# Kernel tuning notes

Hardware: AMD Instinct MI355X
Metric: run time of the kernel (lower is better)

The kernel has to match this reference:

```python
import jax, jax.numpy as jnp
import numpy as np

N_NODES = 100000
N_EDGES = 3200000
IN_FEAT = 128
HIDDEN = 32
NUM_LAYERS = 4
K = 35
NODES_PER_GRAPH = 100


def setup_inputs() -> dict:
    key = jax.random.key(0)
    ks = jax.random.split(key, 20)
    inp = {}
    inp['x'] = jax.random.normal(ks[0], (N_NODES, IN_FEAT), dtype=jnp.float32)
    inp['edge_index'] = jax.random.randint(ks[1], (2, N_EDGES), 0, N_NODES, dtype=jnp.int64)
    inp['batch'] = (jnp.arange(N_NODES, dtype=jnp.int64) // NODES_PER_GRAPH)
    # GCNConv weights (PyG: lin weight [in, out], bias [out])
    dims = [IN_FEAT] + [HIDDEN] * NUM_LAYERS
    for i in range(NUM_LAYERS):
        s = 1.0 / np.sqrt(dims[i])
        inp[f'w{i}'] = jax.random.normal(ks[2 + i], (dims[i], HIDDEN), dtype=jnp.float32) * s
        inp[f'b{i}'] = jnp.zeros((HIDDEN,), dtype=jnp.float32)
    # head: Conv1d(128->16,k=1), Conv1d(16->32,k=5), fc1(416->128), fc2(128->1)
    inp['conv1_w'] = jax.random.normal(ks[8], (16, HIDDEN * NUM_LAYERS, 1), dtype=jnp.float32) * (1.0 / np.sqrt(128))
    inp['conv1_b'] = jnp.zeros((16,), dtype=jnp.float32)
    inp['conv2_w'] = jax.random.normal(ks[9], (32, 16, 5), dtype=jnp.float32) * (1.0 / np.sqrt(16 * 5))
    inp['conv2_b'] = jnp.zeros((32,), dtype=jnp.float32)
    lin_in = 32 * (K // 2 - 4)  # 416
    inp['fc1_w'] = jax.random.normal(ks[10], (128, lin_in), dtype=jnp.float32) * (1.0 / np.sqrt(lin_in))
    inp['fc1_b'] = jnp.zeros((128,), dtype=jnp.float32)
    inp['fc2_w'] = jax.random.normal(ks[11], (1, 128), dtype=jnp.float32) * (1.0 / np.sqrt(128))
    inp['fc2_b'] = jnp.zeros((1,), dtype=jnp.float32)
    return inp


def _gcn_conv(x, w, b, src, dst, n):
    # PyG GCNConv: h = x @ W; add self-loops; sym-normalized scatter-add; + bias
    h = x @ w
    deg = jnp.ones((n,), h.dtype).at[dst].add(1.0)  # degree incl. self-loop
    dis = jax.lax.rsqrt(deg)
    coef = dis[src] * dis[dst]  # [E]
    agg = jax.ops.segment_sum(h[src] * coef[:, None], dst, num_segments=n)
    return agg + h / deg[:, None] + b  # self-loop norm = 1/deg


def reference(x, edge_index, batch, w0, b0, w1, b1, w2, b2, w3, b3,
              conv1_w, conv1_b, conv2_w, conv2_b, fc1_w, fc1_b, fc2_w, fc2_b):
    src, dst = edge_index[0], edge_index[1]
    n = x.shape[0]
    xs = []
    h = x
    for w, b in ((w0, b0), (w1, b1), (w2, b2), (w3, b3)):
        h = jnp.tanh(_gcn_conv(h, w, b, src, dst, n))
        xs.append(h)
    feat = jnp.concatenate(xs, axis=1)  # [N, 128]
    # global_sort_pool: graphs are contiguous blocks of NODES_PER_GRAPH nodes
    G = n // NODES_PER_GRAPH
    dense = feat.reshape(G, NODES_PER_GRAPH, -1)
    order = jnp.argsort(-dense[:, :, -1], axis=1)  # descending by last channel
    topk = jnp.take_along_axis(dense, order[:, :, None], axis=1)[:, :K]  # [G,K,128]
    y = topk.transpose(0, 2, 1)  # [G,128,K]
    y = jax.nn.relu(jnp.einsum('oc,gck->gok', conv1_w[:, :, 0], y) + conv1_b[None, :, None])
    L = y.shape[-1] // 2  # MaxPool1d(2), drop trailing element
    y = y[..., :L * 2].reshape(G, 16, L, 2).max(axis=-1)  # [G,16,17]
    y = jax.lax.conv_general_dilated(y, conv2_w, (1,), 'VALID',
                                     dimension_numbers=('NCH', 'OIH', 'NCH'))
    y = jax.nn.relu(y + conv2_b[None, :, None])  # [G,32,13]
    y = y.reshape(G, -1)  # [G,416]
    y = jax.nn.relu(y @ fc1_w.T + fc1_b)  # dropout is identity in eval
    return jax.nn.sigmoid(y @ fc2_w.T + fc2_b)  # [G,1]
```

## Files before the change

kernel.cpp:

```cpp
#include <hip/hip_runtime.h>
#include <hip/hip_fp16.h>
#include <math.h>

#define N_NODES 100000
#define N_EDGES 3200000
#define HIDDEN 32
#define K_TOP 35
#define NPG 100
#define N_GRAPHS 1000

#define BSHIFT 9
#define NLOC 512
#define NBUCK 196
#define CAP 17408
#define NBB 1024
#define BIN_CHUNK 13


__global__ void k_bin(const int* __restrict__ src, const int* __restrict__ dst,
                      int* __restrict__ bcnt, unsigned int* __restrict__ bdata) {
    __shared__ int h[NBUCK];
    __shared__ int lbase[NBUCK];
    __shared__ int lcur[NBUCK];
    int t = threadIdx.x;
    for (int i = t; i < NBUCK; i += 256) { h[i] = 0; lcur[i] = 0; }
    __syncthreads();
    int base = blockIdx.x * (256 * BIN_CHUNK);
    int ss[BIN_CHUNK], ds[BIN_CHUNK];
#pragma unroll
    for (int k = 0; k < BIN_CHUNK; k++) {
        int e = base + k * 256 + t;
        if (e < N_EDGES) {
            ss[k] = src[e];
            ds[k] = dst[e];
            atomicAdd(&h[ds[k] >> BSHIFT], 1);
        } else ds[k] = -1;
    }
    __syncthreads();
    for (int i = t; i < NBUCK; i += 256)
        lbase[i] = h[i] ? atomicAdd(&bcnt[i], h[i]) : 0;
    __syncthreads();
#pragma unroll
    for (int k = 0; k < BIN_CHUNK; k++) {
        int d = ds[k];
        if (d >= 0) {
            int bk = d >> BSHIFT;
            int pos = atomicAdd(&lcur[bk], 1);
            bdata[bk * CAP + lbase[bk] + pos] =
                ((unsigned int)ss[k] << BSHIFT) | (unsigned int)(d & (NLOC - 1));
        }
    }
}

__global__ void k_build(const unsigned int* __restrict__ bdata, const int* __restrict__ bcnt,
                        int2* __restrict__ rc, float* __restrict__ dis,
                        int* __restrict__ csr) {
    __shared__ int h[NLOC];
    __shared__ int sd[NLOC];
    __shared__ int rp[NLOC];
    __shared__ int cur[NLOC];
    int b = blockIdx.x, t = threadIdx.x;
    if (t < NLOC) h[t] = 0;
    __syncthreads();
    int r0 = b * CAP, r1 = r0 + bcnt[b];
    for (int i = r0 + t; i < r1; i += 1024)
        atomicAdd(&h[bdata[i] & (NLOC - 1)], 1);
    __syncthreads();
    int v = (t < NLOC) ? h[t] : 0;
    if (t < NLOC) sd[t] = v;
    __syncthreads();
    for (int off = 1; off < NLOC; off <<= 1) {
        int x = (t >= off && t < NLOC) ? sd[t - off] : 0;
        __syncthreads();
        if (t < NLOC) sd[t] += x;
        __syncthreads();
    }
    if (t < NLOC) {
        int excl = sd[t] - v;
        int node = (b << BSHIFT) + t;
        rp[t] = r0 + excl;
        cur[t] = 0;
        if (node < N_NODES) {
            rc[node] = make_int2(r0 + excl, v);
            dis[node] = rsqrtf((float)(v + 1));
        }
    }
    __syncthreads();
    for (int i = r0 + t; i < r1; i += 1024) {
        unsigned int u = bdata[i];
        int loc = u & (NLOC - 1);
        int pos = atomicAdd(&cur[loc], 1);
        csr[rp[loc] + pos] = (int)(u >> BSHIFT);
    }
}


__global__ void k_mm0(const float* __restrict__ in, const float* __restrict__ w,
                      const float* __restrict__ dis, char* __restrict__ hs) {
    __shared__ float wl[128 * HIDDEN];
    int t = threadIdx.x;
    for (int i = t; i < 128 * HIDDEN; i += 256) wl[i] = w[i];
    __syncthreads();
    int n0 = blockIdx.x * 512 + t;
    int n1 = n0 + 256;
    bool has0 = n0 < N_NODES, has1 = n1 < N_NODES;
    int m0 = has0 ? n0 : 0, m1 = has1 ? n1 : 0;
    const float* r0p = in + (size_t)m0 * 128;
    const float* r1p = in + (size_t)m1 * 128;
    float acc0[HIDDEN], acc1[HIDDEN];
#pragma unroll
    for (int o = 0; o < HIDDEN; o++) { acc0[o] = 0.f; acc1[o] = 0.f; }
    for (int c4 = 0; c4 < 32; c4++) {
        float4 va = *(const float4*)(r0p + c4 * 4);
        float4 vb = *(const float4*)(r1p + c4 * 4);
        float xa[4] = {va.x, va.y, va.z, va.w};
        float xb[4] = {vb.x, vb.y, vb.z, vb.w};
#pragma unroll
        for (int k = 0; k < 4; k++) {
            const float* wr = &wl[(c4 * 4 + k) * HIDDEN];
#pragma unroll
            for (int o = 0; o < HIDDEN; o++) {
                float wv = wr[o];
                acc0[o] += xa[k] * wv;
                acc1[o] += xb[k] * wv;
            }
        }
    }
    if (has0) {
        float d = dis[m0];
        float4* hr = (float4*)(hs + (size_t)m0 * 64);
#pragma unroll
        for (int qq = 0; qq < 4; qq++) {
            __half2 p[4];
#pragma unroll
            for (int k = 0; k < 4; k++)
                p[k] = __floats2half2_rn(acc0[8 * qq + 2 * k] * d, acc0[8 * qq + 2 * k + 1] * d);
            hr[qq] = *(float4*)p;
        }
    }
    if (has1) {
        float d = dis[m1];
        float4* hr = (float4*)(hs + (size_t)m1 * 64);
#pragma unroll
        for (int qq = 0; qq < 4; qq++) {
            __half2 p[4];
#pragma unroll
            for (int k = 0; k < 4; k++)
                p[k] = __floats2half2_rn(acc1[8 * qq + 2 * k] * d, acc1[8 * qq + 2 * k + 1] * d);
            hr[qq] = *(float4*)p;
        }
    }
}

__global__ void k_agg(const float4* __restrict__ hs4, const float* __restrict__ dis,
                      const int2* __restrict__ rc, const int* __restrict__ csr_src,
                      const float* __restrict__ bias,
                      float* __restrict__ feat, int col_off,
                      const float* __restrict__ wnext, char* __restrict__ hsn) {
    __shared__ float wl[32 * 33];
    __shared__ float tv[8][36];
    int tt = threadIdx.x;
    if (wnext) {
        for (int i = tt; i < 1024; i += 256)
            wl[(i >> 5) * 33 + (i & 31)] = wnext[i];
    }
    __syncthreads();
    int n = (blockIdx.x * 256 + tt) >> 5;
    int c = tt & 31;
    int r = c & 3;
    int ph = c >> 2;
    int slot = tt >> 5;
    int2 rcv = rc[n];
    int start = rcv.x, m = rcv.y;
    float d = dis[n];
    float aA[8] = {0.f, 0.f, 0.f, 0.f, 0.f, 0.f, 0.f, 0.f};
    float aB[8] = {0.f, 0.f, 0.f, 0.f, 0.f, 0.f, 0.f, 0.f};

    for (int base = 0; base < m; base += 32) {
        int e = base + c;
        int idx = (e < m) ? csr_src[start + e] : N_NODES;
        int id0 = __shfl(idx, ph, 32);
        int id1 = __shfl(idx, 8 + ph, 32);
        int id2 = __shfl(idx, 16 + ph, 32);
        int id3 = __shfl(idx, 24 + ph, 32);
        float4 g0 = hs4[(size_t)id0 * 4 + r];
        float4 g1 = hs4[(size_t)id1 * 4 + r];
        float4 g2 = hs4[(size_t)id2 * 4 + r];
        float4 g3 = hs4[(size_t)id3 * 4 + r];
        const __half2* h0 = (const __half2*)&g0;
        const __half2* h1 = (const __half2*)&g1;
        const __half2* h2 = (const __half2*)&g2;
        const __half2* h3 = (const __half2*)&g3;
        float2 f;
#pragma unroll
        for (int j = 0; j < 4; j++) {
            f = __half22float2(h0[j]); aA[2 * j] += f.x; aA[2 * j + 1] += f.y;
        }
#pragma unroll
        for (int j = 0; j < 4; j++) {
            f = __half22float2(h1[j]); aB[2 * j] += f.x; aB[2 * j + 1] += f.y;
        }
#pragma unroll
        for (int j = 0; j < 4; j++) {
            f = __half22float2(h2[j]); aA[2 * j] += f.x; aA[2 * j + 1] += f.y;
        }
#pragma unroll
        for (int j = 0; j < 4; j++) {
            f = __half22float2(h3[j]); aB[2 * j] += f.x; aB[2 * j + 1] += f.y;
        }
    }
    float s[8];
#pragma unroll
    for (int k = 0; k < 8; k++) {
        float v = aA[k] + aB[k];
        v += __shfl_xor(v, 4);
        v += __shfl_xor(v, 8);
        v += __shfl_xor(v, 16);
        s[k] = v;
    }
    float s01 = (ph & 1) ? s[1] : s[0];
    float s23 = (ph & 1) ? s[3] : s[2];
    float s45 = (ph & 1) ? s[5] : s[4];
    float s67 = (ph & 1) ? s[7] : s[6];
    float s03 = (ph & 2) ? s23 : s01;
    float s47 = (ph & 2) ? s67 : s45;
    float sp  = (ph & 4) ? s47 : s03;
    float4 sv = hs4[(size_t)n * 4 + r];
    const __half2* sh = (const __half2*)&sv;
    __half2 q01 = (ph & 2) ? sh[1] : sh[0];
    __half2 q23 = (ph & 2) ? sh[3] : sh[2];
    __half2 qq  = (ph & 4) ? q23 : q01;
    float self = (ph & 1) ? __high2float(qq) : __low2float(qq);
    float bv = bias[8 * r + ph];
    float ov = tanhf(d * (sp + self) + bv);
    __builtin_nontemporal_store(ov, &feat[(size_t)n * 128 + col_off + 8 * r + ph]);
    if (wnext) {
        tv[slot][8 * r + ph] = ov;
        __builtin_amdgcn_wave_barrier();
        float o = 0.f;
#pragma unroll 8
        for (int k = 0; k < 32; k++)
            o += tv[slot][k] * wl[k * 33 + c];
        o *= d;
        float oh = __shfl_xor(o, 1);
        if ((c & 1) == 0) {
            __half2 pck = __floats2half2_rn(o, oh);
            *(__half2*)(hsn + (size_t)n * 64 + (size_t)c * 2) = pck;
        }
    }
}


__global__ void __launch_bounds__(256, 4)
k_head(const float* __restrict__ feat,
       const float* __restrict__ c1w, const float* __restrict__ c1b,
       const float* __restrict__ c2w, const float* __restrict__ c2b,
       const float* __restrict__ f1w, const float* __restrict__ f1b,
       const float* __restrict__ f2w, const float* __restrict__ f2b,
       float* __restrict__ out) {
    __shared__ float vals[NPG];
    __shared__ int sel[K_TOP];
    __shared__ float tk[K_TOP * 132];
    __shared__ float wl1[16 * 129];
    __shared__ float y1[16][36];
    __shared__ float y2[16][17];
    __shared__ float y3[416];
    __shared__ float y4[128];
    __shared__ float r2[128];
    int g = blockIdx.x, t = threadIdx.x;
    const float* fg = feat + (size_t)g * NPG * 128;

    for (int i = t; i < 2048; i += 256)
        wl1[(i >> 7) * 129 + (i & 127)] = c1w[i];
    if (t < NPG) vals[t] = fg[t * 128 + 127];
    __syncthreads();
    if (t < NPG) {
        float v = vals[t];
        int r = 0;
        for (int j = 0; j < NPG; j++) {
            float u = vals[j];
            r += (u > v) || (u == v && j < t);
        }
        if (r < K_TOP) sel[r] = t;
    }
    __syncthreads();
    for (int i = t; i < K_TOP * 32; i += 256) {
        int k = i >> 5, c4 = i & 31;
        *(float4*)&tk[k * 132 + 4 * c4] = *(const float4*)&fg[sel[k] * 128 + 4 * c4];
    }
    __syncthreads();
    for (int i = t; i < 16 * K_TOP; i += 256) {
        int o = i & 15, k = i >> 4;
        float s = c1b[o];
        const float* wr = &wl1[o * 129];
        const float* xr = &tk[k * 132];
#pragma unroll 8
        for (int c = 0; c < 128; c++) s += wr[c] * xr[c];
        y1[o][k] = fmaxf(s, 0.f);
    }
    __syncthreads();
    for (int i = t; i < 16 * 17; i += 256) {
        int o = i & 15, l = i >> 4;
        y2[o][l] = fmaxf(y1[o][2 * l], y1[o][2 * l + 1]);
    }
    __syncthreads();
    for (int idx = t; idx < 32 * 13; idx += 256) {
        int o2 = idx / 13, ttp = idx - o2 * 13;
        float s = c2b[o2];
        const float* wr = c2w + o2 * 80;
#pragma unroll
        for (int i = 0; i < 16; i++)
#pragma unroll
            for (int j = 0; j < 5; j++) s += wr[i * 5 + j] * y2[i][ttp + j];
        y3[idx] = fmaxf(s, 0.f);
    }
    __syncthreads();
    {
        int o = t >> 1, h = t & 1;
        const float4* wr4 = (const float4*)(f1w + o * 416) + h * 52;
        const float* yb = y3 + h * 208;
        float s = 0.f;
#pragma unroll 4
        for (int i = 0; i < 52; i++) {
            float4 w4 = wr4[i];
            s += w4.x * yb[4 * i] + w4.y * yb[4 * i + 1] +
                 w4.z * yb[4 * i + 2] + w4.w * yb[4 * i + 3];
        }
        s += __shfl_xor(s, 1);
        if (h == 0) y4[o] = fmaxf(s + f1b[o], 0.f);
    }
    __syncthreads();
    if (t < 128) r2[t] = f2w[t] * y4[t];
    __syncthreads();
    for (int off = 64; off > 0; off >>= 1) {
        if (t < off) r2[t] += r2[t + off];
        __syncthreads();
    }
    if (t == 0) out[g] = 1.0f / (1.0f + expf(-(r2[0] + f2b[0])));
}


static inline size_t alignup(size_t x) { return (x + 255) & ~(size_t)255; }

extern "C" void kernel_launch(void* const* d_in, const int* in_sizes, int n_in,
                              void* d_out, int out_size, void* d_ws, size_t ws_size,
                              hipStream_t stream) {
    const float* x    = (const float*)d_in[0];
    const int*   ei   = (const int*)d_in[1];
    const int*   srcp = ei;
    const int*   dstp = ei + N_EDGES;
    const float* w0 = (const float*)d_in[3];
    const float* b0 = (const float*)d_in[4];
    const float* w1 = (const float*)d_in[5];
    const float* b1 = (const float*)d_in[6];
    const float* w2 = (const float*)d_in[7];
    const float* b2 = (const float*)d_in[8];
    const float* w3 = (const float*)d_in[9];
    const float* b3 = (const float*)d_in[10];
    const float* c1w = (const float*)d_in[11];
    const float* c1b = (const float*)d_in[12];
    const float* c2w = (const float*)d_in[13];
    const float* c2b = (const float*)d_in[14];
    const float* f1w = (const float*)d_in[15];
    const float* f1b = (const float*)d_in[16];
    const float* f2w = (const float*)d_in[17];
    const float* f2b = (const float*)d_in[18];
    float* out = (float*)d_out;

    char* p = (char*)d_ws;
    int2* rcv    = (int2*)p; p += alignup(sizeof(int2) * N_NODES);
    float* dis   = (float*)p; p += alignup(sizeof(float) * N_NODES);
    int* bcnt    = (int*)p; p += alignup(sizeof(int) * NBUCK);
    int* csr     = (int*)p; p += alignup(sizeof(int) * (size_t)NBUCK * CAP);
    char* U = p;
    unsigned int* bdata = (unsigned int*)U;
    char* hsA = U;
    char* hsB = U + alignup((size_t)N_NODES * 64 + 64);
    size_t usz = alignup(sizeof(unsigned int) * (size_t)NBUCK * CAP);
    float* feat = (float*)(U + usz);

    const int NB_M = (N_NODES + 511) / 512;
    const int NB_A = (N_NODES * 32) / 256;

    hipMemsetAsync(bcnt, 0, sizeof(int) * NBUCK, stream);
    k_bin<<<NBB, 256, 0, stream>>>(srcp, dstp, bcnt, bdata);
    k_build<<<NBUCK, 1024, 0, stream>>>(bdata, bcnt, rcv, dis, csr);

    hipMemsetAsync(hsA + (size_t)N_NODES * 64, 0, 64, stream);
    hipMemsetAsync(hsB + (size_t)N_NODES * 64, 0, 64, stream);

    k_mm0<<<NB_M, 256, 0, stream>>>(x, w0, dis, hsA);
    k_agg<<<NB_A, 256, 0, stream>>>((const float4*)hsA, dis, rcv, csr, b0,
                                    feat, 0, w1, hsB);
    k_agg<<<NB_A, 256, 0, stream>>>((const float4*)hsB, dis, rcv, csr, b1,
                                    feat, 32, w2, hsA);
    k_agg<<<NB_A, 256, 0, stream>>>((const float4*)hsA, dis, rcv, csr, b2,
                                    feat, 64, w3, hsB);
    k_agg<<<NB_A, 256, 0, stream>>>((const float4*)hsB, dis, rcv, csr, b3,
                                    feat, 96, (const float*)nullptr, (char*)nullptr);

    k_head<<<N_GRAPHS, 256, 0, stream>>>(feat, c1w, c1b, c2w, c2b,
                                         f1w, f1b, f2w, f2b, out);
}
```

Measured before the change: 423.3 us.

## Split fp16 hidden features into low/high channel halves and aggregate in two passes

Node features (32 fp16 channels, 64 bytes per node) are now stored as two separate 32-byte arrays holding channels 0-15 and 16-31. The aggregation kernel makes two gather passes over the CSR neighbour list, one per half, so each pass touches a 3.2 MB table that fits better in cache instead of a 6.4 MB one. The trade-off is that the edge indices are read twice and more shuffles and selects are needed to reassemble channels. The zero padding rows for sentinel gathers are now written inside k_mm0, which removes the separate memset calls.

```diff
diff --git a/kernel.cpp b/kernel.cpp
--- a/kernel.cpp
+++ b/kernel.cpp
@@ -96,9 +96,18 @@
 
 
 __global__ void k_mm0(const float* __restrict__ in, const float* __restrict__ w,
-                      const float* __restrict__ dis, char* __restrict__ hs) {
+                      const float* __restrict__ dis,
+                      char* __restrict__ lo, char* __restrict__ hi,
+                      char* __restrict__ loB, char* __restrict__ hiB) {
     __shared__ float wl[128 * HIDDEN];
     int t = threadIdx.x;
+    if (blockIdx.x == 0 && t == 0) {
+        float4 z = make_float4(0.f, 0.f, 0.f, 0.f);
+        float4* p0 = (float4*)(lo  + (size_t)N_NODES * 32); p0[0] = z; p0[1] = z;
+        float4* p1 = (float4*)(hi  + (size_t)N_NODES * 32); p1[0] = z; p1[1] = z;
+        float4* p2 = (float4*)(loB + (size_t)N_NODES * 32); p2[0] = z; p2[1] = z;
+        float4* p3 = (float4*)(hiB + (size_t)N_NODES * 32); p3[0] = z; p3[1] = z;
+    }
     for (int i = t; i < 128 * HIDDEN; i += 256) wl[i] = w[i];
     __syncthreads();
     int n0 = blockIdx.x * 512 + t;
@@ -128,35 +137,39 @@
     }
     if (has0) {
         float d = dis[m0];
-        float4* hr = (float4*)(hs + (size_t)m0 * 64);
+        float4* lr = (float4*)(lo + (size_t)m0 * 32);
+        float4* hr = (float4*)(hi + (size_t)m0 * 32);
 #pragma unroll
         for (int qq = 0; qq < 4; qq++) {
             __half2 p[4];
 #pragma unroll
             for (int k = 0; k < 4; k++)
                 p[k] = __floats2half2_rn(acc0[8 * qq + 2 * k] * d, acc0[8 * qq + 2 * k + 1] * d);
-            hr[qq] = *(float4*)p;
+            if (qq < 2) lr[qq] = *(float4*)p; else hr[qq - 2] = *(float4*)p;
         }
     }
     if (has1) {
         float d = dis[m1];
-        float4* hr = (float4*)(hs + (size_t)m1 * 64);
+        float4* lr = (float4*)(lo + (size_t)m1 * 32);
+        float4* hr = (float4*)(hi + (size_t)m1 * 32);
 #pragma unroll
         for (int qq = 0; qq < 4; qq++) {
             __half2 p[4];
 #pragma unroll
             for (int k = 0; k < 4; k++)
                 p[k] = __floats2half2_rn(acc1[8 * qq + 2 * k] * d, acc1[8 * qq + 2 * k + 1] * d);
-            hr[qq] = *(float4*)p;
-        }
-    }
-}
-
-__global__ void k_agg(const float4* __restrict__ hs4, const float* __restrict__ dis,
+            if (qq < 2) lr[qq] = *(float4*)p; else hr[qq - 2] = *(float4*)p;
+        }
+    }
+}
+
+__global__ void k_agg(const float4* __restrict__ lo, const float4* __restrict__ hi,
+                      const float* __restrict__ dis,
                       const int2* __restrict__ rc, const int* __restrict__ csr_src,
                       const float* __restrict__ bias,
                       float* __restrict__ feat, int col_off,
-                      const float* __restrict__ wnext, char* __restrict__ hsn) {
+                      const float* __restrict__ wnext,
+                      char* __restrict__ loN, char* __restrict__ hiN) {
     __shared__ float wl[32 * 33];
     __shared__ float tv[8][36];
     int tt = threadIdx.x;
@@ -167,85 +180,119 @@
     __syncthreads();
     int n = (blockIdx.x * 256 + tt) >> 5;
     int c = tt & 31;
-    int r = c & 3;
-    int ph = c >> 2;
+    int r = c & 1;
+    int ph = c >> 1;
     int slot = tt >> 5;
     int2 rcv = rc[n];
     int start = rcv.x, m = rcv.y;
     float d = dis[n];
-    float aA[8] = {0.f, 0.f, 0.f, 0.f, 0.f, 0.f, 0.f, 0.f};
-    float aB[8] = {0.f, 0.f, 0.f, 0.f, 0.f, 0.f, 0.f, 0.f};
-
+    float sA[8], sB[8];
+    float acc[8];
+
+#pragma unroll
+    for (int k = 0; k < 8; k++) acc[k] = 0.f;
     for (int base = 0; base < m; base += 32) {
         int e = base + c;
         int idx = (e < m) ? csr_src[start + e] : N_NODES;
         int id0 = __shfl(idx, ph, 32);
-        int id1 = __shfl(idx, 8 + ph, 32);
-        int id2 = __shfl(idx, 16 + ph, 32);
-        int id3 = __shfl(idx, 24 + ph, 32);
-        float4 g0 = hs4[(size_t)id0 * 4 + r];
-        float4 g1 = hs4[(size_t)id1 * 4 + r];
-        float4 g2 = hs4[(size_t)id2 * 4 + r];
-        float4 g3 = hs4[(size_t)id3 * 4 + r];
+        int id1 = __shfl(idx, 16 + ph, 32);
+        float4 g0 = lo[(size_t)id0 * 2 + r];
+        float4 g1 = lo[(size_t)id1 * 2 + r];
         const __half2* h0 = (const __half2*)&g0;
         const __half2* h1 = (const __half2*)&g1;
-        const __half2* h2 = (const __half2*)&g2;
-        const __half2* h3 = (const __half2*)&g3;
         float2 f;
 #pragma unroll
         for (int j = 0; j < 4; j++) {
-            f = __half22float2(h0[j]); aA[2 * j] += f.x; aA[2 * j + 1] += f.y;
+            f = __half22float2(h0[j]); acc[2 * j] += f.x; acc[2 * j + 1] += f.y;
         }
 #pragma unroll
         for (int j = 0; j < 4; j++) {
-            f = __half22float2(h1[j]); aB[2 * j] += f.x; aB[2 * j + 1] += f.y;
-        }
-#pragma unroll
-        for (int j = 0; j < 4; j++) {
-            f = __half22float2(h2[j]); aA[2 * j] += f.x; aA[2 * j + 1] += f.y;
-        }
-#pragma unroll
-        for (int j = 0; j < 4; j++) {
-            f = __half22float2(h3[j]); aB[2 * j] += f.x; aB[2 * j + 1] += f.y;
-        }
-    }
-    float s[8];
+            f = __half22float2(h1[j]); acc[2 * j] += f.x; acc[2 * j + 1] += f.y;
+        }
+    }
 #pragma unroll
     for (int k = 0; k < 8; k++) {
-        float v = aA[k] + aB[k];
+        float v = acc[k];
+        v += __shfl_xor(v, 2);
         v += __shfl_xor(v, 4);
         v += __shfl_xor(v, 8);
         v += __shfl_xor(v, 16);
-        s[k] = v;
-    }
-    float s01 = (ph & 1) ? s[1] : s[0];
-    float s23 = (ph & 1) ? s[3] : s[2];
-    float s45 = (ph & 1) ? s[5] : s[4];
-    float s67 = (ph & 1) ? s[7] : s[6];
-    float s03 = (ph & 2) ? s23 : s01;
-    float s47 = (ph & 2) ? s67 : s45;
-    float sp  = (ph & 4) ? s47 : s03;
-    float4 sv = hs4[(size_t)n * 4 + r];
+        sA[k] = v;
+    }
+
+#pragma unroll
+    for (int k = 0; k < 8; k++) acc[k] = 0.f;
+    for (int base = 0; base < m; base += 32) {
+        int e = base + c;
+        int idx = (e < m) ? csr_src[start + e] : N_NODES;
+        int id0 = __shfl(idx, ph, 32);
+        int id1 = __shfl(idx, 16 + ph, 32);
+        float4 g0 = hi[(size_t)id0 * 2 + r];
+        float4 g1 = hi[(size_t)id1 * 2 + r];
+        const __half2* h0 = (const __half2*)&g0;
+        const __half2* h1 = (const __half2*)&g1;
+        float2 f;
+#pragma unroll
+        for (int j = 0; j < 4; j++) {
+            f = __half22float2(h0[j]); acc[2 * j] += f.x; acc[2 * j + 1] += f.y;
+        }
+#pragma unroll
+        for (int j = 0; j < 4; j++) {
+            f = __half22float2(h1[j]); acc[2 * j] += f.x; acc[2 * j + 1] += f.y;
+        }
+    }
+#pragma unroll
+    for (int k = 0; k < 8; k++) {
+        float v = acc[k];
+        v += __shfl_xor(v, 2);
+        v += __shfl_xor(v, 4);
+        v += __shfl_xor(v, 8);
+        v += __shfl_xor(v, 16);
+        sB[k] = v;
+    }
+
+    int kk = ph & 7;
+    bool loHalf = c < 16;
+    float a01 = (kk & 1) ? sA[1] : sA[0];
+    float a23 = (kk & 1) ? sA[3] : sA[2];
+    float a45 = (kk & 1) ? sA[5] : sA[4];
+    float a67 = (kk & 1) ? sA[7] : sA[6];
+    float a03 = (kk & 2) ? a23 : a01;
+    float a47 = (kk & 2) ? a67 : a45;
+    float ta  = (kk & 4) ? a47 : a03;
+    float b01 = (kk & 1) ? sB[1] : sB[0];
+    float b23 = (kk & 1) ? sB[3] : sB[2];
+    float b45 = (kk & 1) ? sB[5] : sB[4];
+    float b67 = (kk & 1) ? sB[7] : sB[6];
+    float b03 = (kk & 2) ? b23 : b01;
+    float b47 = (kk & 2) ? b67 : b45;
+    float tb  = (kk & 4) ? b47 : b03;
+    float sp  = loHalf ? ta : tb;
+    const float4* sbase = loHalf ? lo : hi;
+    float4 sv = sbase[(size_t)n * 2 + r];
     const __half2* sh = (const __half2*)&sv;
-    __half2 q01 = (ph & 2) ? sh[1] : sh[0];
-    __half2 q23 = (ph & 2) ? sh[3] : sh[2];
-    __half2 qq  = (ph & 4) ? q23 : q01;
-    float self = (ph & 1) ? __high2float(qq) : __low2float(qq);
-    float bv = bias[8 * r + ph];
+    __half2 m01 = (kk & 2) ? sh[1] : sh[0];
+    __half2 m23 = (kk & 2) ? sh[3] : sh[2];
+    __half2 mm  = (kk & 4) ? m23 : m01;
+    float self = (kk & 1) ? __high2float(mm) : __low2float(mm);
+    int q = (c & 1) | ((c >> 4) << 1);
+    int ch = q * 8 + kk;
+    float bv = bias[ch];
     float ov = tanhf(d * (sp + self) + bv);
-    __builtin_nontemporal_store(ov, &feat[(size_t)n * 128 + col_off + 8 * r + ph]);
+    __builtin_nontemporal_store(ov, &feat[(size_t)n * 128 + col_off + ch]);
     if (wnext) {
-        tv[slot][8 * r + ph] = ov;
+        tv[slot][ch] = ov;
         __builtin_amdgcn_wave_barrier();
         float o = 0.f;
 #pragma unroll 8
-        for (int k = 0; k < 32; k++)
-            o += tv[slot][k] * wl[k * 33 + c];
+        for (int k2 = 0; k2 < 32; k2++)
+            o += tv[slot][k2] * wl[k2 * 33 + c];
         o *= d;
         float oh = __shfl_xor(o, 1);
         if ((c & 1) == 0) {
             __half2 pck = __floats2half2_rn(o, oh);
-            *(__half2*)(hsn + (size_t)n * 64 + (size_t)c * 2) = pck;
+            char* dstb = (c < 16) ? loN : hiN;
+            *(__half2*)(dstb + (size_t)n * 32 + (size_t)(c & 15) * 2) = pck;
         }
     }
 }
@@ -374,8 +421,11 @@
     int* csr     = (int*)p; p += alignup(sizeof(int) * (size_t)NBUCK * CAP);
     char* U = p;
     unsigned int* bdata = (unsigned int*)U;
-    char* hsA = U;
-    char* hsB = U + alignup((size_t)N_NODES * 64 + 64);
+    size_t S = alignup((size_t)N_NODES * 32 + 32);
+    char* loA = U;
+    char* hiA = U + S;
+    char* loB = U + 2 * S;
+    char* hiB = U + 3 * S;
     size_t usz = alignup(sizeof(unsigned int) * (size_t)NBUCK * CAP);
     float* feat = (float*)(U + usz);
 
@@ -386,18 +436,16 @@
     k_bin<<<NBB, 256, 0, stream>>>(srcp, dstp, bcnt, bdata);
     k_build<<<NBUCK, 1024, 0, stream>>>(bdata, bcnt, rcv, dis, csr);
 
-    hipMemsetAsync(hsA + (size_t)N_NODES * 64, 0, 64, stream);
-    hipMemsetAsync(hsB + (size_t)N_NODES * 64, 0, 64, stream);
-
-    k_mm0<<<NB_M, 256, 0, stream>>>(x, w0, dis, hsA);
-    k_agg<<<NB_A, 256, 0, stream>>>((const float4*)hsA, dis, rcv, csr, b0,
-                                    feat, 0, w1, hsB);
-    k_agg<<<NB_A, 256, 0, stream>>>((const float4*)hsB, dis, rcv, csr, b1,
-                                    feat, 32, w2, hsA);
-    k_agg<<<NB_A, 256, 0, stream>>>((const float4*)hsA, dis, rcv, csr, b2,
-                                    feat, 64, w3, hsB);
-    k_agg<<<NB_A, 256, 0, stream>>>((const float4*)hsB, dis, rcv, csr, b3,
-                                    feat, 96, (const float*)nullptr, (char*)nullptr);
+    k_mm0<<<NB_M, 256, 0, stream>>>(x, w0, dis, loA, hiA, loB, hiB);
+    k_agg<<<NB_A, 256, 0, stream>>>((const float4*)loA, (const float4*)hiA, dis,
+                                    rcv, csr, b0, feat, 0, w1, loB, hiB);
+    k_agg<<<NB_A, 256, 0, stream>>>((const float4*)loB, (const float4*)hiB, dis,
+                                    rcv, csr, b1, feat, 32, w2, loA, hiA);
+    k_agg<<<NB_A, 256, 0, stream>>>((const float4*)loA, (const float4*)hiA, dis,
+                                    rcv, csr, b2, feat, 64, w3, loB, hiB);
+    k_agg<<<NB_A, 256, 0, stream>>>((const float4*)loB, (const float4*)hiB, dis,
+                                    rcv, csr, b3, feat, 96,
+                                    (const float*)nullptr, (char*)nullptr, (char*)nullptr);
 
     k_head<<<N_GRAPHS, 256, 0, stream>>>(feat, c1w, c1b, c2w, c2b,
                                          f1w, f1b, f2w, f2b, out);
```

Result: slower. 496.8 us (+17.4%).
